# Performance work log

Measured on AMD Instinct MI355X. Metric: run time of the kernel, lower is better.

## Reference

```python
import jax, jax.numpy as jnp
import numpy as np

N_NODES = 50000
N_EDGES = 800000
IN_FEATS = 128
HIDDEN = 128
NUM_CLASSES = 47


def setup_inputs() -> dict:
    key = jax.random.key(0)
    k1, k2, k3, k4 = jax.random.split(key, 4)
    features = jax.random.normal(k1, (N_NODES, IN_FEATS), dtype=jnp.float32)
    edge_index = jax.random.randint(k2, (2, N_EDGES), 0, N_NODES, dtype=jnp.int32)
    # Glorot-style init for weights, zeros for bias (DGL GraphConv defaults)
    W1 = jax.random.normal(k3, (IN_FEATS, HIDDEN), dtype=jnp.float32) * (1.0 / np.sqrt(IN_FEATS))
    b1 = jnp.zeros((HIDDEN,), dtype=jnp.float32)
    W2 = jax.random.normal(k4, (HIDDEN, NUM_CLASSES), dtype=jnp.float32) * (1.0 / np.sqrt(HIDDEN))
    b2 = jnp.zeros((NUM_CLASSES,), dtype=jnp.float32)
    return {"features": features, "edge_index": edge_index,
            "W1": W1, "b1": b1, "W2": W2, "b2": b2}


def _graph_conv(x, W, b, src, dst, norm_src, norm_dst, n_nodes):
    # DGL GraphConv, norm='both': D_dst^{-1/2} A D_src^{-1/2} (X W) + b
    h = (x * norm_src[:, None]) @ W            # transform before aggregation
    agg = jax.ops.segment_sum(h[src], dst, num_segments=n_nodes)
    return agg * norm_dst[:, None] + b


def reference(features, edge_index, W1, b1, W2, b2):
    src, dst = edge_index[0], edge_index[1]
    n = features.shape[0]
    ones = jnp.ones((src.shape[0],), dtype=features.dtype)
    deg_out = jax.ops.segment_sum(ones, src, num_segments=n)
    deg_in = jax.ops.segment_sum(ones, dst, num_segments=n)
    norm_src = jax.lax.rsqrt(jnp.clip(deg_out, 1.0))   # d_out^{-1/2}, clamp >= 1
    norm_dst = jax.lax.rsqrt(jnp.clip(deg_in, 1.0))    # d_in^{-1/2}, clamp >= 1

    h = _graph_conv(features, W1, b1, src, dst, norm_src, norm_dst, n)
    h = jax.nn.relu(h)
    out = _graph_conv(h, W2, b2, src, dst, norm_src, norm_dst, n)
    return out
```

## Files before the change

### kernel.cpp

```cpp
#include <hip/hip_runtime.h>
#include <hip/hip_fp16.h>

#define N_NODES 50000
#define N_EDGES 800000
#define IN_F 128
#define HID 128
#define NCLS 47
#define H2S 48
#define W2C 64
#define NCH 196
#define NB 128
#define CHUNK 6250
#define PDW 12500
#define G1ROWS 256
#define G2ROWS 128


typedef _Float16 f16x8 __attribute__((ext_vector_type(8)));
typedef float f32x4 __attribute__((ext_vector_type(4)));

struct __align__(8)  h2x2 { __half2 a, b; };
struct __align__(16) h2x4 { __half2 a, b, c, d; };

__global__ __launch_bounds__(256) void prep_kernel(const float* __restrict__ W1,
                                                   const float* __restrict__ W2,
                                                   __half* __restrict__ W1Th,
                                                   __half* __restrict__ W1Tl,
                                                   __half* __restrict__ W2Th,
                                                   __half* __restrict__ W2Tl) {
    const int b = blockIdx.x, t = threadIdx.x;
    if (b < 32) {
        const int i0 = b * 512;
        for (int i2 = i0 + t; i2 < i0 + 512; i2 += 256) {
            int cc = i2 >> 7, k = i2 & 127;
            float w = W1[k * HID + cc];
            __half hv = __float2half_rn(w);
            W1Th[i2] = hv;
            W1Tl[i2] = __float2half_rn(w - __half2float(hv));
        }
    } else {
        const int i0 = (b - 32) * 512;
        for (int i2 = i0 + t; i2 < i0 + 512; i2 += 256) {
            int cc = i2 >> 7, k = i2 & 127;
            float w = (cc < NCLS) ? W2[k * NCLS + cc] : 0.f;
            __half hv = __float2half_rn(w);
            W2Th[i2] = hv;
            W2Tl[i2] = __float2half_rn(w - __half2float(hv));
        }
    }
}

__global__ __launch_bounds__(512) void hist_gemm1_kernel(const int* __restrict__ ei,
        unsigned int* __restrict__ Pdst, unsigned int* __restrict__ Psrc,
        const float* __restrict__ X, const __half* __restrict__ W1Th,
        const __half* __restrict__ W1Tl, __half* __restrict__ H1h) {
    __shared__ unsigned int h[PDW];
    const int t = threadIdx.x;
    if (blockIdx.x < 2 * NB) {
        const bool is_src = blockIdx.x >= NB;
        const int chunk = blockIdx.x & (NB - 1);
        const int* ids = is_src ? ei : ei + N_EDGES;
        uint2* h2 = (uint2*)h;
        for (int j = t; j < PDW / 2; j += 512) h2[j] = make_uint2(0u, 0u);
        __syncthreads();
        const int e0 = chunk * CHUNK;
        const int2* e2p = (const int2*)(ids + e0);
        for (int k = t; k < CHUNK / 2; k += 512) {
            int2 v2 = e2p[k];
            atomicAdd(&h[v2.x >> 2], 1u << ((v2.x & 3) * 8));
            atomicAdd(&h[v2.y >> 2], 1u << ((v2.y & 3) * 8));
        }
        __syncthreads();
        unsigned int* P = (is_src ? Psrc : Pdst) + (size_t)chunk * PDW;
        uint2* P2 = (uint2*)P;
        for (int j = t; j < PDW / 2; j += 512) P2[j] = h2[j];
    } else {
        const int lane = t & 63;
        const int wv = t >> 6;
        const int r16 = lane & 15;
        const int kg = lane >> 4;
        const int row0 = (blockIdx.x - 2 * NB) * G1ROWS + wv * 32;
        f32x4 acc[2][8] = {};
#pragma unroll
        for (int s = 0; s < 4; ++s) {
            const int k0 = 32 * s + 8 * kg;
            f16x8 ah[2], al[2];
#pragma unroll
            for (int rt = 0; rt < 2; ++rt) {
                int row = row0 + rt * 16 + r16;
                int rc = row < N_NODES ? row : N_NODES - 1;
                const float4 x0 = *(const float4*)&X[(size_t)rc * IN_F + k0];
                const float4 x1 = *(const float4*)&X[(size_t)rc * IN_F + k0 + 4];
                const float xv[8] = {x0.x, x0.y, x0.z, x0.w,
                                     x1.x, x1.y, x1.z, x1.w};
#pragma unroll
                for (int j = 0; j < 8; ++j) {
                    _Float16 hv = (_Float16)xv[j];
                    ah[rt][j] = hv;
                    al[rt][j] = (_Float16)(xv[j] - (float)hv);
                }
            }
#pragma unroll
            for (int tt = 0; tt < 8; ++tt) {
                const f16x8 bh = *(const f16x8*)&W1Th[(16 * tt + r16) * IN_F + k0];
                const f16x8 bl = *(const f16x8*)&W1Tl[(16 * tt + r16) * IN_F + k0];
#pragma unroll
                for (int rt = 0; rt < 2; ++rt) {
                    acc[rt][tt] = __builtin_amdgcn_mfma_f32_16x16x32_f16(
                        ah[rt], bh, acc[rt][tt], 0, 0, 0);
                    acc[rt][tt] = __builtin_amdgcn_mfma_f32_16x16x32_f16(
                        al[rt], bh, acc[rt][tt], 0, 0, 0);
                    acc[rt][tt] = __builtin_amdgcn_mfma_f32_16x16x32_f16(
                        ah[rt], bl, acc[rt][tt], 0, 0, 0);
                }
            }
        }
#pragma unroll
        for (int rt = 0; rt < 2; ++rt)
#pragma unroll
            for (int j = 0; j < 4; ++j) {
                const int row = row0 + rt * 16 + 4 * kg + j;
                if (row < N_NODES) {
#pragma unroll
                    for (int tt = 0; tt < 8; ++tt)
                        H1h[(size_t)row * HID + 16 * tt + r16] =
                            __float2half_rn(acc[rt][tt][j]);
                }
            }
    }
}

__global__ __launch_bounds__(256) void reduce_kernel(unsigned int* __restrict__ Pdst,
                                                     const unsigned int* __restrict__ Psrc,
                                                     int* __restrict__ cnt_in,
                                                     float* __restrict__ norm_src,
                                                     float* __restrict__ norm_dst,
                                                     int* __restrict__ chunk_sums) {
    __shared__ int sm[256];
    const int t = threadIdx.x;
    const int j = blockIdx.x * 256 + t;
    int tot = 0;
    if (j < PDW) {
        unsigned int run = 0;
#pragma unroll 8
        for (int b = 0; b < NB; ++b) {
            unsigned int v = Pdst[(size_t)b * PDW + j];
            Pdst[(size_t)b * PDW + j] = run;
            run += v;
        }
        int n0 = run & 0xff, n1 = (run >> 8) & 0xff;
        int n2 = (run >> 16) & 0xff, n3 = (run >> 24) & 0xff;
        *(int4*)&cnt_in[4 * j] = make_int4(n0, n1, n2, n3);
        *(float4*)&norm_dst[4 * j] = make_float4(
            rsqrtf(fmaxf((float)n0, 1.0f)), rsqrtf(fmaxf((float)n1, 1.0f)),
            rsqrtf(fmaxf((float)n2, 1.0f)), rsqrtf(fmaxf((float)n3, 1.0f)));
        tot = n0 + n1 + n2 + n3;
        unsigned int rs = 0;
#pragma unroll 8
        for (int b = 0; b < NB; ++b) rs += Psrc[(size_t)b * PDW + j];
        int s0 = rs & 0xff, s1 = (rs >> 8) & 0xff;
        int s2 = (rs >> 16) & 0xff, s3 = (rs >> 24) & 0xff;
        *(float4*)&norm_src[4 * j] = make_float4(
            rsqrtf(fmaxf((float)s0, 1.0f)), rsqrtf(fmaxf((float)s1, 1.0f)),
            rsqrtf(fmaxf((float)s2, 1.0f)), rsqrtf(fmaxf((float)s3, 1.0f)));
    }
    sm[t] = tot;
    __syncthreads();
    const int g = t & 63;
    for (int off = 32; off > 0; off >>= 1) {
        if (g < off) sm[t] += sm[t + off];
        __syncthreads();
    }
    if (g == 0) chunk_sums[blockIdx.x * 4 + (t >> 6)] = sm[t];
}

__global__ __launch_bounds__(256) void scan3_kernel(const int* __restrict__ cnt_in,
                                                    const int* __restrict__ chunk_sums,
                                                    int* __restrict__ offsets) {
    __shared__ int sm[256];
    const int t = threadIdx.x;
    int v = (t < NCH) ? chunk_sums[t] : 0;
    sm[t] = v;
    __syncthreads();
    for (int off = 1; off < 256; off <<= 1) {
        int u = (t >= off) ? sm[t - off] : 0;
        __syncthreads();
        sm[t] += u;
        __syncthreads();
    }
    const int basev = (blockIdx.x == 0) ? 0 : sm[blockIdx.x - 1];
    __syncthreads();
    const int idx = blockIdx.x * 256 + t;
    int c = (idx < N_NODES) ? cnt_in[idx] : 0;
    sm[t] = c;
    __syncthreads();
    for (int off = 1; off < 256; off <<= 1) {
        int u = (t >= off) ? sm[t - off] : 0;
        __syncthreads();
        sm[t] += u;
        __syncthreads();
    }
    if (idx < N_NODES) offsets[idx] = basev + sm[t] - c;
    if (blockIdx.x == 0 && t == 0) offsets[N_NODES] = N_EDGES;
}

__global__ __launch_bounds__(512) void fill_kernel(const int* __restrict__ src,
        const int* __restrict__ dst, const int* __restrict__ offsets,
        const unsigned int* __restrict__ Pdst, int* __restrict__ csr_src) {
    __shared__ __align__(16) unsigned int cur[PDW];
    const int t = threadIdx.x;
    const int chunk = blockIdx.x;
    uint2* c2 = (uint2*)cur;
    for (int j = t; j < PDW / 2; j += 512) c2[j] = make_uint2(0u, 0u);
    __syncthreads();
    const unsigned int* base = Pdst + (size_t)chunk * PDW;
    const int e0 = chunk * CHUNK;
    const int2* d2p = (const int2*)(dst + e0);
    const int2* s2p = (const int2*)(src + e0);
    for (int k = t; k < CHUNK / 2; k += 512) {
        int2 d2 = d2p[k];
        int2 s2 = s2p[k];
        {
            const int d = d2.x;
            const int sh = (d & 3) * 8;
            const unsigned int bw = base[d >> 2];
            const int off = offsets[d];
            unsigned int old = atomicAdd(&cur[d >> 2], 1u << sh);
            csr_src[off + (int)((bw >> sh) & 0xffu) + (int)((old >> sh) & 0xffu)] = s2.x;
        }
        {
            const int d = d2.y;
            const int sh = (d & 3) * 8;
            const unsigned int bw = base[d >> 2];
            const int off = offsets[d];
            unsigned int old = atomicAdd(&cur[d >> 2], 1u << sh);
            csr_src[off + (int)((bw >> sh) & 0xffu) + (int)((old >> sh) & 0xffu)] = s2.y;
        }
    }
}

__global__ __launch_bounds__(256) void gather1_kernel(const __half* __restrict__ H1h,
        const int* __restrict__ offsets, const int* __restrict__ csr_src,
        const float* __restrict__ b1, const float* __restrict__ norm_src,
        const float* __restrict__ norm_dst, __half* __restrict__ Hrelu16) {
    const int lane = threadIdx.x & 63;
    const int q = lane >> 4;
    const int fl = lane & 15;
    const int row = blockIdx.x * 4 + (threadIdx.x >> 6);
    const int beg = offsets[row], end = offsets[row + 1];
    float a0 = 0.f, a1 = 0.f, a2 = 0.f, a3 = 0.f;
    float a4 = 0.f, a5 = 0.f, a6 = 0.f, a7 = 0.f;
    for (int base = beg; base < end; base += 64) {
        int idx = 0;
        float nsv = 0.f;
        if (base + lane < end) {
            idx = csr_src[base + lane];
            nsv = norm_src[idx];
        }
        const int cnt = min(end - base, 64);
        for (int j = 0; j < cnt; j += 16) {
            int e0 = j + q, e1 = j + 4 + q, e2 = j + 8 + q, e3 = j + 12 + q;
            int s0 = __shfl(idx, e0);  float n0 = __shfl(nsv, e0);
            int s1 = __shfl(idx, e1);  float n1 = __shfl(nsv, e1);
            int s2 = __shfl(idx, e2);  float n2 = __shfl(nsv, e2);
            int s3 = __shfl(idx, e3);  float n3 = __shfl(nsv, e3);
            h2x4 v0 = *(const h2x4*)&H1h[(size_t)s0 * HID + 8 * fl];
            h2x4 v1 = *(const h2x4*)&H1h[(size_t)s1 * HID + 8 * fl];
            h2x4 v2 = *(const h2x4*)&H1h[(size_t)s2 * HID + 8 * fl];
            h2x4 v3 = *(const h2x4*)&H1h[(size_t)s3 * HID + 8 * fl];
            float2 f;
            f = __half22float2(v0.a); a0 = fmaf(f.x, n0, a0); a1 = fmaf(f.y, n0, a1);
            f = __half22float2(v0.b); a2 = fmaf(f.x, n0, a2); a3 = fmaf(f.y, n0, a3);
            f = __half22float2(v0.c); a4 = fmaf(f.x, n0, a4); a5 = fmaf(f.y, n0, a5);
            f = __half22float2(v0.d); a6 = fmaf(f.x, n0, a6); a7 = fmaf(f.y, n0, a7);
            f = __half22float2(v1.a); a0 = fmaf(f.x, n1, a0); a1 = fmaf(f.y, n1, a1);
            f = __half22float2(v1.b); a2 = fmaf(f.x, n1, a2); a3 = fmaf(f.y, n1, a3);
            f = __half22float2(v1.c); a4 = fmaf(f.x, n1, a4); a5 = fmaf(f.y, n1, a5);
            f = __half22float2(v1.d); a6 = fmaf(f.x, n1, a6); a7 = fmaf(f.y, n1, a7);
            f = __half22float2(v2.a); a0 = fmaf(f.x, n2, a0); a1 = fmaf(f.y, n2, a1);
            f = __half22float2(v2.b); a2 = fmaf(f.x, n2, a2); a3 = fmaf(f.y, n2, a3);
            f = __half22float2(v2.c); a4 = fmaf(f.x, n2, a4); a5 = fmaf(f.y, n2, a5);
            f = __half22float2(v2.d); a6 = fmaf(f.x, n2, a6); a7 = fmaf(f.y, n2, a7);
            f = __half22float2(v3.a); a0 = fmaf(f.x, n3, a0); a1 = fmaf(f.y, n3, a1);
            f = __half22float2(v3.b); a2 = fmaf(f.x, n3, a2); a3 = fmaf(f.y, n3, a3);
            f = __half22float2(v3.c); a4 = fmaf(f.x, n3, a4); a5 = fmaf(f.y, n3, a5);
            f = __half22float2(v3.d); a6 = fmaf(f.x, n3, a6); a7 = fmaf(f.y, n3, a7);
        }
    }
    a0 += __shfl_xor(a0, 16); a1 += __shfl_xor(a1, 16);
    a2 += __shfl_xor(a2, 16); a3 += __shfl_xor(a3, 16);
    a4 += __shfl_xor(a4, 16); a5 += __shfl_xor(a5, 16);
    a6 += __shfl_xor(a6, 16); a7 += __shfl_xor(a7, 16);
    a0 += __shfl_xor(a0, 32); a1 += __shfl_xor(a1, 32);
    a2 += __shfl_xor(a2, 32); a3 += __shfl_xor(a3, 32);
    a4 += __shfl_xor(a4, 32); a5 += __shfl_xor(a5, 32);
    a6 += __shfl_xor(a6, 32); a7 += __shfl_xor(a7, 32);
    if (lane < 16) {
        float nd = norm_dst[row], ns = norm_src[row];
        float4 bA = *(const float4*)&b1[8 * fl];
        float4 bB = *(const float4*)&b1[8 * fl + 4];
        float o0 = fmaxf(fmaf(a0, nd, bA.x), 0.f) * ns;
        float o1 = fmaxf(fmaf(a1, nd, bA.y), 0.f) * ns;
        float o2 = fmaxf(fmaf(a2, nd, bA.z), 0.f) * ns;
        float o3 = fmaxf(fmaf(a3, nd, bA.w), 0.f) * ns;
        float o4 = fmaxf(fmaf(a4, nd, bB.x), 0.f) * ns;
        float o5 = fmaxf(fmaf(a5, nd, bB.y), 0.f) * ns;
        float o6 = fmaxf(fmaf(a6, nd, bB.z), 0.f) * ns;
        float o7 = fmaxf(fmaf(a7, nd, bB.w), 0.f) * ns;
        h2x4 p = {__floats2half2_rn(o0, o1), __floats2half2_rn(o2, o3),
                  __floats2half2_rn(o4, o5), __floats2half2_rn(o6, o7)};
        *(h2x4*)&Hrelu16[(size_t)row * HID + 8 * fl] = p;
    }
}

__global__ __launch_bounds__(256) void gemm2_kernel(const __half* __restrict__ Hrelu16,
                                                    const __half* __restrict__ W2Th,
                                                    const __half* __restrict__ W2Tl,
                                                    __half* __restrict__ H2h) {
    const int lane = threadIdx.x & 63;
    const int wv = threadIdx.x >> 6;
    const int r16 = lane & 15;
    const int kg = lane >> 4;
    const int row0 = blockIdx.x * G2ROWS + wv * 32;
    f32x4 acc[2][3] = {};
#pragma unroll
    for (int s = 0; s < 4; ++s) {
        const int k0 = 32 * s + 8 * kg;
        f16x8 a[2];
#pragma unroll
        for (int rt = 0; rt < 2; ++rt) {
            int row = row0 + rt * 16 + r16;
            int rc = row < N_NODES ? row : N_NODES - 1;
            a[rt] = *(const f16x8*)&Hrelu16[(size_t)rc * HID + k0];
        }
#pragma unroll
        for (int tt = 0; tt < 3; ++tt) {
            const f16x8 bh = *(const f16x8*)&W2Th[(16 * tt + r16) * HID + k0];
            const f16x8 bl = *(const f16x8*)&W2Tl[(16 * tt + r16) * HID + k0];
#pragma unroll
            for (int rt = 0; rt < 2; ++rt) {
                acc[rt][tt] = __builtin_amdgcn_mfma_f32_16x16x32_f16(
                    a[rt], bh, acc[rt][tt], 0, 0, 0);
                acc[rt][tt] = __builtin_amdgcn_mfma_f32_16x16x32_f16(
                    a[rt], bl, acc[rt][tt], 0, 0, 0);
            }
        }
    }
#pragma unroll
    for (int rt = 0; rt < 2; ++rt)
#pragma unroll
        for (int j = 0; j < 4; ++j) {
            const int row = row0 + rt * 16 + 4 * kg + j;
            if (row < N_NODES) {
#pragma unroll
                for (int tt = 0; tt < 3; ++tt)
                    H2h[(size_t)row * H2S + 16 * tt + r16] =
                        __float2half_rn(acc[rt][tt][j]);
            }
        }
}

__global__ __launch_bounds__(256) void gather2_kernel(const __half* __restrict__ H2h,
        const int* __restrict__ offsets, const int* __restrict__ csr_src,
        const float* __restrict__ b2, const float* __restrict__ norm_dst,
        float* __restrict__ out) {
    const int lane = threadIdx.x & 63;
    const int row = blockIdx.x * 4 + (threadIdx.x >> 6);
    const int beg = offsets[row], end = offsets[row + 1];
    const int cl = min(lane, H2S - 1);
    float acc = 0.f;
    for (int base = beg; base < end; base += 64) {
        int idx = 0;
        float wv = 0.f;
        if (base + lane < end) {
            idx = csr_src[base + lane];
            wv = 1.f;
        }
        const int cnt = min(end - base, 64);
        for (int j = 0; j < cnt; j += 4) {
            int s0 = __shfl(idx, j);     float w0 = __shfl(wv, j);
            int s1 = __shfl(idx, j + 1); float w1 = __shfl(wv, j + 1);
            int s2 = __shfl(idx, j + 2); float w2 = __shfl(wv, j + 2);
            int s3 = __shfl(idx, j + 3); float w3 = __shfl(wv, j + 3);
            float f0 = __half2float(H2h[(size_t)s0 * H2S + cl]);
            float f1 = __half2float(H2h[(size_t)s1 * H2S + cl]);
            float f2 = __half2float(H2h[(size_t)s2 * H2S + cl]);
            float f3 = __half2float(H2h[(size_t)s3 * H2S + cl]);
            acc = fmaf(f0, w0, acc);
            acc = fmaf(f1, w1, acc);
            acc = fmaf(f2, w2, acc);
            acc = fmaf(f3, w3, acc);
        }
    }
    if (lane < NCLS) out[(size_t)row * NCLS + lane] = acc * norm_dst[row] + b2[lane];
}

extern "C" void kernel_launch(void* const* d_in, const int* in_sizes, int n_in,
                              void* d_out, int out_size, void* d_ws, size_t ws_size,
                              hipStream_t stream) {
    const float* X  = (const float*)d_in[0];
    const int*   ei = (const int*)d_in[1];
    const float* W1 = (const float*)d_in[2];
    const float* b1 = (const float*)d_in[3];
    const float* W2 = (const float*)d_in[4];
    const float* b2 = (const float*)d_in[5];
    float* out = (float*)d_out;

    const int* src = ei;
    const int* dst = ei + N_EDGES;

    char* w = (char*)d_ws;
    auto alloc = [&](size_t bytes) {
        char* p = w;
        w += (bytes + 255) & ~(size_t)255;
        return p;
    };
    float*  norm_src   = (float*)alloc(N_NODES * 4);
    float*  norm_dst   = (float*)alloc(N_NODES * 4);
    int*    cnt_in     = (int*)alloc(N_NODES * 4);
    int*    offsets    = (int*)alloc((N_NODES + 1) * 4);
    int*    csr_src    = (int*)alloc((size_t)N_EDGES * 4);
    int*    chunk_sums = (int*)alloc(NCH * 4);
    __half* W1Th       = (__half*)alloc((size_t)IN_F * HID * 2);
    __half* W1Tl       = (__half*)alloc((size_t)IN_F * HID * 2);
    __half* W2Th       = (__half*)alloc((size_t)W2C * HID * 2);
    __half* W2Tl       = (__half*)alloc((size_t)W2C * HID * 2);
    __half* H1h        = (__half*)alloc((size_t)N_NODES * HID * 2);
    __half* Hrelu16    = (__half*)alloc((size_t)N_NODES * HID * 2);
    __half* H2h        = (__half*)alloc((size_t)N_NODES * H2S * 2);
    unsigned int* Pdst = (unsigned int*)alloc((size_t)NB * PDW * 4);
    unsigned int* Psrc = (unsigned int*)alloc((size_t)NB * PDW * 4);

    const int g1_blocks = (N_NODES + G1ROWS - 1) / G1ROWS;
    const int g2_blocks = (N_NODES + G2ROWS - 1) / G2ROWS;
    prep_kernel<<<48, 256, 0, stream>>>(W1, W2, W1Th, W1Tl, W2Th, W2Tl);
    hist_gemm1_kernel<<<2 * NB + g1_blocks, 512, 0, stream>>>(ei, Pdst, Psrc,
                                                              X, W1Th, W1Tl, H1h);
    reduce_kernel<<<(PDW + 255) / 256, 256, 0, stream>>>(Pdst, Psrc, cnt_in,
                                                         norm_src, norm_dst, chunk_sums);
    scan3_kernel<<<NCH, 256, 0, stream>>>(cnt_in, chunk_sums, offsets);
    fill_kernel<<<NB, 512, 0, stream>>>(src, dst, offsets, Pdst, csr_src);
    gather1_kernel<<<N_NODES / 4, 256, 0, stream>>>(H1h, offsets, csr_src, b1,
                                                    norm_src, norm_dst, Hrelu16);
    gemm2_kernel<<<g2_blocks, 256, 0, stream>>>(Hrelu16, W2Th, W2Tl, H2h);
    gather2_kernel<<<N_NODES / 4, 256, 0, stream>>>(H2h, offsets, csr_src, b2,
                                                    norm_dst, out);
}
```

Baseline: 207.2 us.

## Fuse reduce+scan via grid barrier and fuse gather1 with gemm2

Merges the degree reduce and the offset scan into one kernel of 98 co-resident blocks that synchronise through a global atomic counter, with block 0 scanning the per-block totals. It also fuses the layer-1 gather/ReLU with the layer-2 MFMA GEMM: 16 aggregated rows are staged in shared memory and multiplied by W2 directly, so the Hrelu16 round trip through global memory and two kernel launches go away. The cost is a spin-wait grid barrier that relies on all blocks being resident at once, and lower parallelism in the gather stage, since each wave now processes two rows in sequence.

```diff
diff --git a/kernel.cpp b/kernel.cpp
--- a/kernel.cpp
+++ b/kernel.cpp
@@ -7,13 +7,12 @@
 #define HID 128
 #define NCLS 47
 #define H2S 48
-#define W2C 64
-#define NCH 196
 #define NB 128
 #define CHUNK 6250
 #define PDW 12500
 #define G1ROWS 256
-#define G2ROWS 128
+#define RSB 98
+#define RSC 128
 
 
 typedef _Float16 f16x8 __attribute__((ext_vector_type(8)));
@@ -27,7 +26,8 @@
                                                    __half* __restrict__ W1Th,
                                                    __half* __restrict__ W1Tl,
                                                    __half* __restrict__ W2Th,
-                                                   __half* __restrict__ W2Tl) {
+                                                   __half* __restrict__ W2Tl,
+                                                   int* __restrict__ sync) {
     const int b = blockIdx.x, t = threadIdx.x;
     if (b < 32) {
         const int i0 = b * 512;
@@ -38,7 +38,7 @@
             W1Th[i2] = hv;
             W1Tl[i2] = __float2half_rn(w - __half2float(hv));
         }
-    } else {
+    } else if (b < 48) {
         const int i0 = (b - 32) * 512;
         for (int i2 = i0 + t; i2 < i0 + 512; i2 += 256) {
             int cc = i2 >> 7, k = i2 & 127;
@@ -47,6 +47,8 @@
             W2Th[i2] = hv;
             W2Tl[i2] = __float2half_rn(w - __half2float(hv));
         }
+    } else {
+        if (t < 2) sync[t] = 0;
     }
 }
 
@@ -130,57 +132,83 @@
     }
 }
 
-__global__ __launch_bounds__(256) void reduce_kernel(unsigned int* __restrict__ Pdst,
-                                                     const unsigned int* __restrict__ Psrc,
-                                                     int* __restrict__ cnt_in,
-                                                     float* __restrict__ norm_src,
-                                                     float* __restrict__ norm_dst,
-                                                     int* __restrict__ chunk_sums) {
+__global__ __launch_bounds__(256) void reduce_scan_kernel(
+        unsigned int* __restrict__ Pdst, const unsigned int* __restrict__ Psrc,
+        float* __restrict__ norm_src, float* __restrict__ norm_dst,
+        int* __restrict__ offsets, int* __restrict__ chunk_sums,
+        int* __restrict__ chunk_base, int* __restrict__ sync) {
     __shared__ int sm[256];
     const int t = threadIdx.x;
-    const int j = blockIdx.x * 256 + t;
-    int tot = 0;
-    if (j < PDW) {
-        unsigned int run = 0;
+    const int b = blockIdx.x;
+    const int j = b * RSC + t;
+    unsigned int run = 0;
+    int n0 = 0, n1 = 0, n2 = 0, n3 = 0, tot = 0;
+    if (t < RSC && j < PDW) {
 #pragma unroll 8
-        for (int b = 0; b < NB; ++b) {
-            unsigned int v = Pdst[(size_t)b * PDW + j];
-            Pdst[(size_t)b * PDW + j] = run;
+        for (int c = 0; c < NB; ++c) {
+            unsigned int v = Pdst[(size_t)c * PDW + j];
+            Pdst[(size_t)c * PDW + j] = run;
             run += v;
         }
-        int n0 = run & 0xff, n1 = (run >> 8) & 0xff;
-        int n2 = (run >> 16) & 0xff, n3 = (run >> 24) & 0xff;
-        *(int4*)&cnt_in[4 * j] = make_int4(n0, n1, n2, n3);
+        n0 = run & 0xff; n1 = (run >> 8) & 0xff;
+        n2 = (run >> 16) & 0xff; n3 = (run >> 24) & 0xff;
+        tot = n0 + n1 + n2 + n3;
         *(float4*)&norm_dst[4 * j] = make_float4(
             rsqrtf(fmaxf((float)n0, 1.0f)), rsqrtf(fmaxf((float)n1, 1.0f)),
             rsqrtf(fmaxf((float)n2, 1.0f)), rsqrtf(fmaxf((float)n3, 1.0f)));
-        tot = n0 + n1 + n2 + n3;
         unsigned int rs = 0;
 #pragma unroll 8
-        for (int b = 0; b < NB; ++b) rs += Psrc[(size_t)b * PDW + j];
+        for (int c = 0; c < NB; ++c) rs += Psrc[(size_t)c * PDW + j];
         int s0 = rs & 0xff, s1 = (rs >> 8) & 0xff;
         int s2 = (rs >> 16) & 0xff, s3 = (rs >> 24) & 0xff;
         *(float4*)&norm_src[4 * j] = make_float4(
             rsqrtf(fmaxf((float)s0, 1.0f)), rsqrtf(fmaxf((float)s1, 1.0f)),
             rsqrtf(fmaxf((float)s2, 1.0f)), rsqrtf(fmaxf((float)s3, 1.0f)));
     }
-    sm[t] = tot;
-    __syncthreads();
-    const int g = t & 63;
+    sm[t] = (t < RSC) ? tot : 0;
+    __syncthreads();
     for (int off = 32; off > 0; off >>= 1) {
-        if (g < off) sm[t] += sm[t + off];
-        __syncthreads();
-    }
-    if (g == 0) chunk_sums[blockIdx.x * 4 + (t >> 6)] = sm[t];
-}
-
-__global__ __launch_bounds__(256) void scan3_kernel(const int* __restrict__ cnt_in,
-                                                    const int* __restrict__ chunk_sums,
-                                                    int* __restrict__ offsets) {
-    __shared__ int sm[256];
-    const int t = threadIdx.x;
-    int v = (t < NCH) ? chunk_sums[t] : 0;
-    sm[t] = v;
+        if ((t & 63) < off) sm[t] += sm[t + off];
+        __syncthreads();
+    }
+    if (t == 0)  atomicExch(&chunk_sums[2 * b], sm[0]);
+    if (t == 64) atomicExch(&chunk_sums[2 * b + 1], sm[64]);
+    __threadfence();
+    __syncthreads();
+    if (t == 0) atomicAdd(&sync[0], 1);
+    if (b == 0) {
+        if (t == 0) {
+            while (atomicAdd(&sync[0], 0) < RSB) __builtin_amdgcn_s_sleep(8);
+        }
+        __syncthreads();
+        __threadfence();
+        int v = (t < 2 * RSB) ? atomicAdd(&chunk_sums[t], 0) : 0;
+        sm[t] = v;
+        __syncthreads();
+        for (int off = 1; off < 256; off <<= 1) {
+            int u = (t >= off) ? sm[t - off] : 0;
+            __syncthreads();
+            sm[t] += u;
+            __syncthreads();
+        }
+        if (t < 2 * RSB) atomicExch(&chunk_base[t], sm[t] - v);
+        __threadfence();
+        __syncthreads();
+        if (t == 0) {
+            offsets[N_NODES] = N_EDGES;
+            atomicExch(&sync[1], 1);
+        }
+    }
+    if (t == 0) {
+        while (atomicAdd(&sync[1], 0) == 0) __builtin_amdgcn_s_sleep(8);
+    }
+    __syncthreads();
+    __threadfence();
+    if (t == 0) sm[0] = atomicAdd(&chunk_base[2 * b], 0);
+    __syncthreads();
+    const int E = sm[0];
+    __syncthreads();
+    sm[t] = (t < RSC) ? tot : 0;
     __syncthreads();
     for (int off = 1; off < 256; off <<= 1) {
         int u = (t >= off) ? sm[t - off] : 0;
@@ -188,20 +216,12 @@
         sm[t] += u;
         __syncthreads();
     }
-    const int basev = (blockIdx.x == 0) ? 0 : sm[blockIdx.x - 1];
-    __syncthreads();
-    const int idx = blockIdx.x * 256 + t;
-    int c = (idx < N_NODES) ? cnt_in[idx] : 0;
-    sm[t] = c;
-    __syncthreads();
-    for (int off = 1; off < 256; off <<= 1) {
-        int u = (t >= off) ? sm[t - off] : 0;
-        __syncthreads();
-        sm[t] += u;
-        __syncthreads();
-    }
-    if (idx < N_NODES) offsets[idx] = basev + sm[t] - c;
-    if (blockIdx.x == 0 && t == 0) offsets[N_NODES] = N_EDGES;
+    if (t < RSC && j < PDW) {
+        const int base0 = E + sm[t] - tot;
+        *(int4*)&offsets[4 * j] = make_int4(base0, base0 + n0,
+                                            base0 + n0 + n1,
+                                            base0 + n0 + n1 + n2);
+    }
 }
 
 __global__ __launch_bounds__(512) void fill_kernel(const int* __restrict__ src,
@@ -239,125 +259,106 @@
     }
 }
 
-__global__ __launch_bounds__(256) void gather1_kernel(const __half* __restrict__ H1h,
-        const int* __restrict__ offsets, const int* __restrict__ csr_src,
-        const float* __restrict__ b1, const float* __restrict__ norm_src,
-        const float* __restrict__ norm_dst, __half* __restrict__ Hrelu16) {
-    const int lane = threadIdx.x & 63;
+__global__ __launch_bounds__(512) void gather1_gemm2_kernel(
+        const __half* __restrict__ H1h, const int* __restrict__ offsets,
+        const int* __restrict__ csr_src, const float* __restrict__ b1,
+        const float* __restrict__ norm_src, const float* __restrict__ norm_dst,
+        const __half* __restrict__ W2Th, const __half* __restrict__ W2Tl,
+        __half* __restrict__ H2h) {
+    __shared__ __align__(16) __half As[16][136];
+    const int t = threadIdx.x;
+    const int lane = t & 63;
+    const int w = t >> 6;
     const int q = lane >> 4;
     const int fl = lane & 15;
-    const int row = blockIdx.x * 4 + (threadIdx.x >> 6);
-    const int beg = offsets[row], end = offsets[row + 1];
-    float a0 = 0.f, a1 = 0.f, a2 = 0.f, a3 = 0.f;
-    float a4 = 0.f, a5 = 0.f, a6 = 0.f, a7 = 0.f;
-    for (int base = beg; base < end; base += 64) {
-        int idx = 0;
-        float nsv = 0.f;
-        if (base + lane < end) {
-            idx = csr_src[base + lane];
-            nsv = norm_src[idx];
-        }
-        const int cnt = min(end - base, 64);
-        for (int j = 0; j < cnt; j += 16) {
-            int e0 = j + q, e1 = j + 4 + q, e2 = j + 8 + q, e3 = j + 12 + q;
-            int s0 = __shfl(idx, e0);  float n0 = __shfl(nsv, e0);
-            int s1 = __shfl(idx, e1);  float n1 = __shfl(nsv, e1);
-            int s2 = __shfl(idx, e2);  float n2 = __shfl(nsv, e2);
-            int s3 = __shfl(idx, e3);  float n3 = __shfl(nsv, e3);
-            h2x4 v0 = *(const h2x4*)&H1h[(size_t)s0 * HID + 8 * fl];
-            h2x4 v1 = *(const h2x4*)&H1h[(size_t)s1 * HID + 8 * fl];
-            h2x4 v2 = *(const h2x4*)&H1h[(size_t)s2 * HID + 8 * fl];
-            h2x4 v3 = *(const h2x4*)&H1h[(size_t)s3 * HID + 8 * fl];
-            float2 f;
-            f = __half22float2(v0.a); a0 = fmaf(f.x, n0, a0); a1 = fmaf(f.y, n0, a1);
-            f = __half22float2(v0.b); a2 = fmaf(f.x, n0, a2); a3 = fmaf(f.y, n0, a3);
-            f = __half22float2(v0.c); a4 = fmaf(f.x, n0, a4); a5 = fmaf(f.y, n0, a5);
-            f = __half22float2(v0.d); a6 = fmaf(f.x, n0, a6); a7 = fmaf(f.y, n0, a7);
-            f = __half22float2(v1.a); a0 = fmaf(f.x, n1, a0); a1 = fmaf(f.y, n1, a1);
-            f = __half22float2(v1.b); a2 = fmaf(f.x, n1, a2); a3 = fmaf(f.y, n1, a3);
-            f = __half22float2(v1.c); a4 = fmaf(f.x, n1, a4); a5 = fmaf(f.y, n1, a5);
-            f = __half22float2(v1.d); a6 = fmaf(f.x, n1, a6); a7 = fmaf(f.y, n1, a7);
-            f = __half22float2(v2.a); a0 = fmaf(f.x, n2, a0); a1 = fmaf(f.y, n2, a1);
-            f = __half22float2(v2.b); a2 = fmaf(f.x, n2, a2); a3 = fmaf(f.y, n2, a3);
-            f = __half22float2(v2.c); a4 = fmaf(f.x, n2, a4); a5 = fmaf(f.y, n2, a5);
-            f = __half22float2(v2.d); a6 = fmaf(f.x, n2, a6); a7 = fmaf(f.y, n2, a7);
-            f = __half22float2(v3.a); a0 = fmaf(f.x, n3, a0); a1 = fmaf(f.y, n3, a1);
-            f = __half22float2(v3.b); a2 = fmaf(f.x, n3, a2); a3 = fmaf(f.y, n3, a3);
-            f = __half22float2(v3.c); a4 = fmaf(f.x, n3, a4); a5 = fmaf(f.y, n3, a5);
-            f = __half22float2(v3.d); a6 = fmaf(f.x, n3, a6); a7 = fmaf(f.y, n3, a7);
-        }
-    }
-    a0 += __shfl_xor(a0, 16); a1 += __shfl_xor(a1, 16);
-    a2 += __shfl_xor(a2, 16); a3 += __shfl_xor(a3, 16);
-    a4 += __shfl_xor(a4, 16); a5 += __shfl_xor(a5, 16);
-    a6 += __shfl_xor(a6, 16); a7 += __shfl_xor(a7, 16);
-    a0 += __shfl_xor(a0, 32); a1 += __shfl_xor(a1, 32);
-    a2 += __shfl_xor(a2, 32); a3 += __shfl_xor(a3, 32);
-    a4 += __shfl_xor(a4, 32); a5 += __shfl_xor(a5, 32);
-    a6 += __shfl_xor(a6, 32); a7 += __shfl_xor(a7, 32);
-    if (lane < 16) {
-        float nd = norm_dst[row], ns = norm_src[row];
-        float4 bA = *(const float4*)&b1[8 * fl];
-        float4 bB = *(const float4*)&b1[8 * fl + 4];
-        float o0 = fmaxf(fmaf(a0, nd, bA.x), 0.f) * ns;
-        float o1 = fmaxf(fmaf(a1, nd, bA.y), 0.f) * ns;
-        float o2 = fmaxf(fmaf(a2, nd, bA.z), 0.f) * ns;
-        float o3 = fmaxf(fmaf(a3, nd, bA.w), 0.f) * ns;
-        float o4 = fmaxf(fmaf(a4, nd, bB.x), 0.f) * ns;
-        float o5 = fmaxf(fmaf(a5, nd, bB.y), 0.f) * ns;
-        float o6 = fmaxf(fmaf(a6, nd, bB.z), 0.f) * ns;
-        float o7 = fmaxf(fmaf(a7, nd, bB.w), 0.f) * ns;
-        h2x4 p = {__floats2half2_rn(o0, o1), __floats2half2_rn(o2, o3),
-                  __floats2half2_rn(o4, o5), __floats2half2_rn(o6, o7)};
-        *(h2x4*)&Hrelu16[(size_t)row * HID + 8 * fl] = p;
-    }
-}
-
-__global__ __launch_bounds__(256) void gemm2_kernel(const __half* __restrict__ Hrelu16,
-                                                    const __half* __restrict__ W2Th,
-                                                    const __half* __restrict__ W2Tl,
-                                                    __half* __restrict__ H2h) {
-    const int lane = threadIdx.x & 63;
-    const int wv = threadIdx.x >> 6;
-    const int r16 = lane & 15;
-    const int kg = lane >> 4;
-    const int row0 = blockIdx.x * G2ROWS + wv * 32;
-    f32x4 acc[2][3] = {};
-#pragma unroll
-    for (int s = 0; s < 4; ++s) {
-        const int k0 = 32 * s + 8 * kg;
-        f16x8 a[2];
-#pragma unroll
-        for (int rt = 0; rt < 2; ++rt) {
-            int row = row0 + rt * 16 + r16;
-            int rc = row < N_NODES ? row : N_NODES - 1;
-            a[rt] = *(const f16x8*)&Hrelu16[(size_t)rc * HID + k0];
-        }
-#pragma unroll
-        for (int tt = 0; tt < 3; ++tt) {
-            const f16x8 bh = *(const f16x8*)&W2Th[(16 * tt + r16) * HID + k0];
-            const f16x8 bl = *(const f16x8*)&W2Tl[(16 * tt + r16) * HID + k0];
-#pragma unroll
-            for (int rt = 0; rt < 2; ++rt) {
-                acc[rt][tt] = __builtin_amdgcn_mfma_f32_16x16x32_f16(
-                    a[rt], bh, acc[rt][tt], 0, 0, 0);
-                acc[rt][tt] = __builtin_amdgcn_mfma_f32_16x16x32_f16(
-                    a[rt], bl, acc[rt][tt], 0, 0, 0);
+    const int row0 = blockIdx.x * 16;
+    for (int rr = 0; rr < 2; ++rr) {
+        const int lr = 2 * w + rr;
+        const int row = row0 + lr;
+        const int beg = offsets[row], end = offsets[row + 1];
+        float a0 = 0.f, a1 = 0.f, a2 = 0.f, a3 = 0.f;
+        float a4 = 0.f, a5 = 0.f, a6 = 0.f, a7 = 0.f;
+        for (int base = beg; base < end; base += 64) {
+            int idx = 0;
+            float nsv = 0.f;
+            if (base + lane < end) {
+                idx = csr_src[base + lane];
+                nsv = norm_src[idx];
             }
-        }
-    }
-#pragma unroll
-    for (int rt = 0; rt < 2; ++rt)
-#pragma unroll
-        for (int j = 0; j < 4; ++j) {
-            const int row = row0 + rt * 16 + 4 * kg + j;
-            if (row < N_NODES) {
-#pragma unroll
-                for (int tt = 0; tt < 3; ++tt)
-                    H2h[(size_t)row * H2S + 16 * tt + r16] =
-                        __float2half_rn(acc[rt][tt][j]);
+            const int cnt = min(end - base, 64);
+            for (int j = 0; j < cnt; j += 16) {
+                int e0 = j + q, e1 = j + 4 + q, e2 = j + 8 + q, e3 = j + 12 + q;
+                int s0 = __shfl(idx, e0);  float n0 = __shfl(nsv, e0);
+                int s1 = __shfl(idx, e1);  float n1 = __shfl(nsv, e1);
+                int s2 = __shfl(idx, e2);  float n2 = __shfl(nsv, e2);
+                int s3 = __shfl(idx, e3);  float n3 = __shfl(nsv, e3);
+                h2x4 v0 = *(const h2x4*)&H1h[(size_t)s0 * HID + 8 * fl];
+                h2x4 v1 = *(const h2x4*)&H1h[(size_t)s1 * HID + 8 * fl];
+                h2x4 v2 = *(const h2x4*)&H1h[(size_t)s2 * HID + 8 * fl];
+                h2x4 v3 = *(const h2x4*)&H1h[(size_t)s3 * HID + 8 * fl];
+                float2 f;
+                f = __half22float2(v0.a); a0 = fmaf(f.x, n0, a0); a1 = fmaf(f.y, n0, a1);
+                f = __half22float2(v0.b); a2 = fmaf(f.x, n0, a2); a3 = fmaf(f.y, n0, a3);
+                f = __half22float2(v0.c); a4 = fmaf(f.x, n0, a4); a5 = fmaf(f.y, n0, a5);
+                f = __half22float2(v0.d); a6 = fmaf(f.x, n0, a6); a7 = fmaf(f.y, n0, a7);
+                f = __half22float2(v1.a); a0 = fmaf(f.x, n1, a0); a1 = fmaf(f.y, n1, a1);
+                f = __half22float2(v1.b); a2 = fmaf(f.x, n1, a2); a3 = fmaf(f.y, n1, a3);
+                f = __half22float2(v1.c); a4 = fmaf(f.x, n1, a4); a5 = fmaf(f.y, n1, a5);
+                f = __half22float2(v1.d); a6 = fmaf(f.x, n1, a6); a7 = fmaf(f.y, n1, a7);
+                f = __half22float2(v2.a); a0 = fmaf(f.x, n2, a0); a1 = fmaf(f.y, n2, a1);
+                f = __half22float2(v2.b); a2 = fmaf(f.x, n2, a2); a3 = fmaf(f.y, n2, a3);
+                f = __half22float2(v2.c); a4 = fmaf(f.x, n2, a4); a5 = fmaf(f.y, n2, a5);
+                f = __half22float2(v2.d); a6 = fmaf(f.x, n2, a6); a7 = fmaf(f.y, n2, a7);
+                f = __half22float2(v3.a); a0 = fmaf(f.x, n3, a0); a1 = fmaf(f.y, n3, a1);
+                f = __half22float2(v3.b); a2 = fmaf(f.x, n3, a2); a3 = fmaf(f.y, n3, a3);
+                f = __half22float2(v3.c); a4 = fmaf(f.x, n3, a4); a5 = fmaf(f.y, n3, a5);
+                f = __half22float2(v3.d); a6 = fmaf(f.x, n3, a6); a7 = fmaf(f.y, n3, a7);
             }
         }
+        a0 += __shfl_xor(a0, 16); a1 += __shfl_xor(a1, 16);
+        a2 += __shfl_xor(a2, 16); a3 += __shfl_xor(a3, 16);
+        a4 += __shfl_xor(a4, 16); a5 += __shfl_xor(a5, 16);
+        a6 += __shfl_xor(a6, 16); a7 += __shfl_xor(a7, 16);
+        a0 += __shfl_xor(a0, 32); a1 += __shfl_xor(a1, 32);
+        a2 += __shfl_xor(a2, 32); a3 += __shfl_xor(a3, 32);
+        a4 += __shfl_xor(a4, 32); a5 += __shfl_xor(a5, 32);
+        a6 += __shfl_xor(a6, 32); a7 += __shfl_xor(a7, 32);
+        if (lane < 16) {
+            float nd = norm_dst[row], ns = norm_src[row];
+            float4 bA = *(const float4*)&b1[8 * fl];
+            float4 bB = *(const float4*)&b1[8 * fl + 4];
+            float o0 = fmaxf(fmaf(a0, nd, bA.x), 0.f) * ns;
+            float o1 = fmaxf(fmaf(a1, nd, bA.y), 0.f) * ns;
+            float o2 = fmaxf(fmaf(a2, nd, bA.z), 0.f) * ns;
+            float o3 = fmaxf(fmaf(a3, nd, bA.w), 0.f) * ns;
+            float o4 = fmaxf(fmaf(a4, nd, bB.x), 0.f) * ns;
+            float o5 = fmaxf(fmaf(a5, nd, bB.y), 0.f) * ns;
+            float o6 = fmaxf(fmaf(a6, nd, bB.z), 0.f) * ns;
+            float o7 = fmaxf(fmaf(a7, nd, bB.w), 0.f) * ns;
+            h2x4 p = {__floats2half2_rn(o0, o1), __floats2half2_rn(o2, o3),
+                      __floats2half2_rn(o4, o5), __floats2half2_rn(o6, o7)};
+            *(h2x4*)&As[lr][8 * fl] = p;
+        }
+    }
+    __syncthreads();
+    if (w < 3) {
+        const int r16 = lane & 15;
+        const int kg = lane >> 4;
+        f32x4 acc = {};
+#pragma unroll
+        for (int s = 0; s < 4; ++s) {
+            const int k0 = 32 * s + 8 * kg;
+            const f16x8 a = *(const f16x8*)&As[r16][k0];
+            const f16x8 bh = *(const f16x8*)&W2Th[(16 * w + r16) * HID + k0];
+            const f16x8 bl = *(const f16x8*)&W2Tl[(16 * w + r16) * HID + k0];
+            acc = __builtin_amdgcn_mfma_f32_16x16x32_f16(a, bh, acc, 0, 0, 0);
+            acc = __builtin_amdgcn_mfma_f32_16x16x32_f16(a, bl, acc, 0, 0, 0);
+        }
+#pragma unroll
+        for (int jj = 0; jj < 4; ++jj)
+            H2h[(size_t)(row0 + 4 * kg + jj) * H2S + 16 * w + r16] =
+                __float2half_rn(acc[jj]);
+    }
 }
 
 __global__ __launch_bounds__(256) void gather2_kernel(const __half* __restrict__ H2h,
@@ -417,32 +418,31 @@
     };
     float*  norm_src   = (float*)alloc(N_NODES * 4);
     float*  norm_dst   = (float*)alloc(N_NODES * 4);
-    int*    cnt_in     = (int*)alloc(N_NODES * 4);
     int*    offsets    = (int*)alloc((N_NODES + 1) * 4);
     int*    csr_src    = (int*)alloc((size_t)N_EDGES * 4);
-    int*    chunk_sums = (int*)alloc(NCH * 4);
+    int*    chunk_sums = (int*)alloc(2 * RSB * 4);
+    int*    chunk_base = (int*)alloc(2 * RSB * 4);
+    int*    syncw      = (int*)alloc(2 * 4);
     __half* W1Th       = (__half*)alloc((size_t)IN_F * HID * 2);
     __half* W1Tl       = (__half*)alloc((size_t)IN_F * HID * 2);
-    __half* W2Th       = (__half*)alloc((size_t)W2C * HID * 2);
-    __half* W2Tl       = (__half*)alloc((size_t)W2C * HID * 2);
+    __half* W2Th       = (__half*)alloc((size_t)64 * HID * 2);
+    __half* W2Tl       = (__half*)alloc((size_t)64 * HID * 2);
     __half* H1h        = (__half*)alloc((size_t)N_NODES * HID * 2);
-    __half* Hrelu16    = (__half*)alloc((size_t)N_NODES * HID * 2);
     __half* H2h        = (__half*)alloc((size_t)N_NODES * H2S * 2);
     unsigned int* Pdst = (unsigned int*)alloc((size_t)NB * PDW * 4);
     unsigned int* Psrc = (unsigned int*)alloc((size_t)NB * PDW * 4);
 
     const int g1_blocks = (N_NODES + G1ROWS - 1) / G1ROWS;
-    const int g2_blocks = (N_NODES + G2ROWS - 1) / G2ROWS;
-    prep_kernel<<<48, 256, 0, stream>>>(W1, W2, W1Th, W1Tl, W2Th, W2Tl);
+    prep_kernel<<<49, 256, 0, stream>>>(W1, W2, W1Th, W1Tl, W2Th, W2Tl, syncw);
     hist_gemm1_kernel<<<2 * NB + g1_blocks, 512, 0, stream>>>(ei, Pdst, Psrc,
                                                               X, W1Th, W1Tl, H1h);
-    reduce_kernel<<<(PDW + 255) / 256, 256, 0, stream>>>(Pdst, Psrc, cnt_in,
-                                                         norm_src, norm_dst, chunk_sums);
-    scan3_kernel<<<NCH, 256, 0, stream>>>(cnt_in, chunk_sums, offsets);
+    reduce_scan_kernel<<<RSB, 256, 0, stream>>>(Pdst, Psrc, norm_src, norm_dst,
+                                                offsets, chunk_sums, chunk_base,
+                                                syncw);
     fill_kernel<<<NB, 512, 0, stream>>>(src, dst, offsets, Pdst, csr_src);
-    gather1_kernel<<<N_NODES / 4, 256, 0, stream>>>(H1h, offsets, csr_src, b1,
-                                                    norm_src, norm_dst, Hrelu16);
-    gemm2_kernel<<<g2_blocks, 256, 0, stream>>>(Hrelu16, W2Th, W2Tl, H2h);
+    gather1_gemm2_kernel<<<N_NODES / 16, 512, 0, stream>>>(H1h, offsets, csr_src,
+                                                           b1, norm_src, norm_dst,
+                                                           W2Th, W2Tl, H2h);
     gather2_kernel<<<N_NODES / 4, 256, 0, stream>>>(H2h, offsets, csr_src, b2,
                                                     norm_dst, out);
 }
```

After: 221.5 us. 6.9% more time.
